# Kernel optimization log

Hardware: AMD Instinct MI355X
Metric: run time of the kernel (lower is better)

Reference implementation:

```python
import jax, jax.numpy as jnp
import numpy as np

N, H, HEADS, SLICES = 200000, 256, 8, 64
DH = H // HEADS  # 32


def setup_inputs() -> dict:
    key = jax.random.key(0)
    ks = jax.random.split(key, 13)
    r = lambda k, shape, scale: jax.random.normal(k, shape, dtype=jnp.float32) * scale
    return {
        "x": r(ks[0], (N, H), 1.0),
        "Wx": r(ks[1], (H, H), H ** -0.5),
        "bx": r(ks[2], (H,), 0.02),
        "Wfx": r(ks[3], (H, H), H ** -0.5),
        "bfx": r(ks[4], (H,), 0.02),
        "Wslice": r(ks[5], (SLICES, DH), DH ** -0.5),
        "bslice": r(ks[6], (SLICES,), 0.02),
        "Wq": r(ks[7], (DH, DH), DH ** -0.5),
        "Wk": r(ks[8], (DH, DH), DH ** -0.5),
        "Wv": r(ks[9], (DH, DH), DH ** -0.5),
        "Wout": r(ks[10], (H, H), H ** -0.5),
        "bout": r(ks[11], (H,), 0.02),
        "temperature": jnp.full((HEADS, 1, 1), 0.5, dtype=jnp.float32),
    }


def reference(x, Wx, bx, Wfx, bfx, Wslice, bslice, Wq, Wk, Wv, Wout, bout, temperature):
    n, hidden = x.shape
    heads, dh = HEADS, DH
    scale = dh ** -0.5

    def to_heads(y):  # (n, hidden) -> (heads, n, dh)
        return jnp.transpose(y.reshape(n, heads, dh), (1, 0, 2))

    fx_mid = to_heads(x @ Wfx.T + bfx)              # (h, n, d)
    x_mid = to_heads(x @ Wx.T + bx)                 # (h, n, d)

    temp = jnp.clip(temperature, 0.1, 5.0)          # (h, 1, 1)
    slice_logits = (jnp.einsum('hnd,gd->hng', x_mid, Wslice) + bslice) / temp
    slice_weights = jax.nn.softmax(slice_logits, axis=-1)   # (h, n, g)
    slice_norm = jnp.sum(slice_weights, axis=1)              # (h, g)

    slice_token = jnp.einsum('hnc,hng->hgc', fx_mid, slice_weights)
    slice_token = slice_token / (slice_norm[:, :, None] + 1e-05)  # (h, g, d)

    q = jnp.einsum('hgd,ed->hge', slice_token, Wq)
    k = jnp.einsum('hgd,ed->hge', slice_token, Wk)
    v = jnp.einsum('hgd,ed->hge', slice_token, Wv)

    dots = jnp.einsum('hgd,hkd->hgk', q, k) * scale
    attn = jax.nn.softmax(dots, axis=-1)
    out_slice = jnp.einsum('hgk,hkd->hgd', attn, v)          # (h, g, d)

    out_x = jnp.einsum('hgc,hng->hnc', out_slice, slice_weights)  # (h, n, d)
    out_x = jnp.transpose(out_x, (1, 0, 2)).reshape(n, hidden)
    return out_x @ Wout.T + bout
```

## Files before the change

kernel.cpp:

```cpp
#include <hip/hip_runtime.h>

typedef unsigned short u16;
typedef __attribute__((ext_vector_type(2))) unsigned int u32x2;
typedef __attribute__((ext_vector_type(4))) unsigned int u32x4;
typedef __attribute__((ext_vector_type(4))) float f32x4;
typedef __attribute__((ext_vector_type(8))) short bf16x8;

__device__ __forceinline__ float bf2f(u16 u) {
    union { unsigned int i; float f; } v; v.i = ((unsigned int)u) << 16; return v.f;
}
__device__ __forceinline__ u16 f2bf(float f) {
    union { float f; unsigned int i; } v; v.f = f;
    unsigned int x = v.i;
    return (u16)((x + 0x7fffu + ((x >> 16) & 1u)) >> 16);
}
__device__ __forceinline__ unsigned int pack2(float a, float b) {
    return (unsigned int)f2bf(a) | ((unsigned int)f2bf(b) << 16);
}
__device__ __forceinline__ void split2(float a, float b, unsigned int& h, unsigned int& l) {
    u16 ha = f2bf(a), hb = f2bf(b);
    u16 la = f2bf(a - bf2f(ha)), lb = f2bf(b - bf2f(hb));
    h = (unsigned int)ha | ((unsigned int)hb << 16);
    l = (unsigned int)la | ((unsigned int)lb << 16);
}
__device__ __forceinline__ void tsplit2(float a, float b,
                                        unsigned int& h, unsigned int& l) {
    unsigned int ua = __float_as_uint(a), ub = __float_as_uint(b);
    float fa = __uint_as_float(ua & 0xffff0000u);
    float fb = __uint_as_float(ub & 0xffff0000u);
    h = (ua >> 16) | (ub & 0xffff0000u);
    float la = a - fa, lb = b - fb;
    l = (__float_as_uint(la) >> 16) | (__float_as_uint(lb) & 0xffff0000u);
}

__device__ __forceinline__ f32x4 MFMA(bf16x8 a, bf16x8 b, f32x4 c) {
    return __builtin_amdgcn_mfma_f32_16x16x32_bf16(a, b, c, 0, 0, 0);
}

__global__ __launch_bounds__(256) void kprep(
    const float* __restrict__ Wx, const float* __restrict__ Wfx,
    const float* __restrict__ Wslice, const float* __restrict__ bslice,
    const float* __restrict__ temperature,
    u16* __restrict__ WxTb, u16* __restrict__ WfxTg,
    u16* __restrict__ WsP, float* __restrict__ bslv)
{
    const int gidx = blockIdx.x * 256 + threadIdx.x;
    if (gidx < 65536) {
        WxTb[gidx] = f2bf(Wx[gidx]);
    } else if (gidx < 131072) {
        const int i = gidx - 65536;
        WfxTg[i] = f2bf(Wfx[i]);
    } else if (gidx < 147456) {
        const int i = gidx - 131072;
        const int h = i >> 11;
        const int rem = i & 2047;
        const int gfc = rem >> 9;
        const int l = (rem >> 3) & 63;
        const int j = i & 7;
        const int g = gfc * 16 + (l & 15);
        const int d = ((j >> 2) << 4) + ((l >> 4) << 2) + (j & 3);
        float tc = fminf(fmaxf(temperature[h], 0.1f), 5.0f);
        WsP[i] = f2bf(Wslice[g * 32 + d] / tc);
    } else if (gidx < 147968) {
        const int i = gidx - 147456;
        const int h = i >> 6, g = i & 63;
        float tc = fminf(fmaxf(temperature[h], 0.1f), 5.0f);
        bslv[i] = bslice[g] / tc;
    }
}

#define LDS_XH 65536
#define LDS_XL 98304
#define LDS_IM 131072
__global__ __launch_bounds__(512, 2) void kAB(
    const float* __restrict__ x, const u16* __restrict__ WxTb,
    const u16* __restrict__ WfxTg, const u16* __restrict__ WsP,
    const float* __restrict__ bx, const float* __restrict__ bfx,
    const float* __restrict__ bslv,
    u16* __restrict__ swg, float* __restrict__ pst, float* __restrict__ pnorm)
{
    __shared__ char lds[147456];
    const int tid  = threadIdx.x;
    const int wv   = tid >> 6;
    const int lane = tid & 63;
    const int l15  = lane & 15;
    const int l4   = lane >> 4;
    const int hl   = wv >> 2;
    const int tq   = wv & 3;

    const int bid  = blockIdx.x;
    const int c    = bid >> 2;
    const int hp   = bid & 3;
    const int head = hp * 2 + hl;

    for (int u = tid; u < 4096; u += 512) {
        const int row = u >> 5, seg = u & 31;
        const u16* src;
        if (row < 64)
            src = WxTb + ((size_t)(hp * 2 + (row >> 5)) * 32 + (row & 31)) * 256 + seg * 8;
        else {
            const int rr = row - 64;
            src = WfxTg + ((size_t)(hp * 2 + (rr >> 5)) * 32 + (rr & 31)) * 256 + seg * 8;
        }
        *(u32x4*)(lds + ((row * 512 + seg * 16) ^ ((row & 7) << 4))) = *(const u32x4*)src;
    }

    bf16x8 wsp[4];
    #pragma unroll
    for (int g = 0; g < 4; ++g)
        wsp[g] = *(const bf16x8*)(WsP + (size_t)head * 2048 + g * 512 + lane * 8);
    float bsl[4], bfv[2], bxv[2][4];
    #pragma unroll
    for (int g = 0; g < 4; ++g) bsl[g] = bslv[head * 64 + g * 16 + l15];
    #pragma unroll
    for (int fc = 0; fc < 2; ++fc) bfv[fc] = bfx[head * 32 + fc * 16 + l15];
    #pragma unroll
    for (int fc = 0; fc < 2; ++fc)
        #pragma unroll
        for (int r = 0; r < 4; ++r)
            bxv[fc][r] = bx[head * 32 + fc * 16 + l4 * 4 + r];

    f32x4 stacc[2][4];
    #pragma unroll
    for (int i = 0; i < 2; ++i)
        #pragma unroll
        for (int j = 0; j < 4; ++j) stacc[i][j] = (f32x4){0.f, 0.f, 0.f, 0.f};
    float nacc[4] = {0.f, 0.f, 0.f, 0.f};

    const int cnt = 12 + (c < 53 ? 1 : 0);
    const long tb = (long)c * 12 + (c < 53 ? c : 53);

    const int row = tid >> 3, seg = tid & 7;
    const int xswz = (row & 7) << 4;

    f32x4 pf[8];
    #pragma unroll
    for (int i = 0; i < 8; ++i)
        pf[i] = *(const f32x4*)(x + (size_t)(tb * 64 + row) * 256 + i * 32 + seg * 4);

    const int xrow = tq * 16 + l15;
    const int xoff = xrow * 512;
    const int xkey = (xrow & 7) << 4;

    for (int t = 0; t < cnt; ++t) {
        const long tok0 = (tb + t) * 64;

        #pragma unroll
        for (int i = 0; i < 8; ++i) {
            unsigned int h0, l0, h1, l1;
            split2(pf[i][0], pf[i][1], h0, l0);
            split2(pf[i][2], pf[i][3], h1, l1);
            const int a = (row * 512 + i * 64 + seg * 8) ^ xswz;
            *(u32x2*)(lds + LDS_XH + a) = (u32x2){h0, h1};
            *(u32x2*)(lds + LDS_XL + a) = (u32x2){l0, l1};
        }
        __syncthreads();

        f32x4 acc1[2], accF[2];
        #pragma unroll
        for (int fc = 0; fc < 2; ++fc) {
            accF[fc] = (f32x4){bfv[fc], bfv[fc], bfv[fc], bfv[fc]};
            acc1[fc] = (f32x4){0.f, 0.f, 0.f, 0.f};
        }
        #pragma unroll
        for (int ks = 0; ks < 8; ++ks) {
            const int kb = ks * 64 + l4 * 16;
            bf16x8 ah = *(const bf16x8*)(lds + LDS_XH + ((xoff + kb) ^ xkey));
            bf16x8 al = *(const bf16x8*)(lds + LDS_XL + ((xoff + kb) ^ xkey));
            bf16x8 awx[2], awf[2];
            #pragma unroll
            for (int fc = 0; fc < 2; ++fc) {
                const int r1 = hl * 32 + fc * 16 + l15;
                awx[fc] = *(const bf16x8*)(lds + ((r1 * 512 + kb) ^ ((r1 & 7) << 4)));
                const int r2 = 64 + r1;
                awf[fc] = *(const bf16x8*)(lds + ((r2 * 512 + kb) ^ ((r2 & 7) << 4)));
            }
            #pragma unroll
            for (int fc = 0; fc < 2; ++fc) {
                accF[fc] = MFMA(ah, awf[fc], accF[fc]);
                acc1[fc] = MFMA(awx[fc], ah, acc1[fc]);
                acc1[fc] = MFMA(awx[fc], al, acc1[fc]);
            }
        }

        if (t + 1 < cnt) {
            #pragma unroll
            for (int i = 0; i < 8; ++i)
                pf[i] = *(const f32x4*)(x + (size_t)(tok0 + 64 + row) * 256 + i * 32 + seg * 4);
        }

        union { u32x4 u; bf16x8 b; } a2h, a2l;
        {
            unsigned int h0, l0, h1, l1, h2, l2, h3, l3;
            float m0 = acc1[0][0] + bxv[0][0];
            float m1 = acc1[0][1] + bxv[0][1];
            float m2 = acc1[0][2] + bxv[0][2];
            float m3 = acc1[0][3] + bxv[0][3];
            tsplit2(m0, m1, h0, l0);
            tsplit2(m2, m3, h1, l1);
            float n0 = acc1[1][0] + bxv[1][0];
            float n1 = acc1[1][1] + bxv[1][1];
            float n2 = acc1[1][2] + bxv[1][2];
            float n3 = acc1[1][3] + bxv[1][3];
            tsplit2(n0, n1, h2, l2);
            tsplit2(n2, n3, h3, l3);
            a2h.u = (u32x4){h0, h1, h2, h3};
            a2l.u = (u32x4){l0, l1, l2, l3};
        }
        f32x4 accL[4];
        #pragma unroll
        for (int g = 0; g < 4; ++g) {
            accL[g] = (f32x4){bsl[g], bsl[g], bsl[g], bsl[g]};
            accL[g] = MFMA(a2h.b, wsp[g], accL[g]);
            accL[g] = MFMA(a2l.b, wsp[g], accL[g]);
        }

        float mrow[4], srow4[4];
        #pragma unroll
        for (int r = 0; r < 4; ++r)
            mrow[r] = fmaxf(fmaxf(accL[0][r], accL[1][r]), fmaxf(accL[2][r], accL[3][r]));
        #pragma unroll
        for (int d = 1; d <= 8; d <<= 1)
            #pragma unroll
            for (int r = 0; r < 4; ++r)
                mrow[r] = fmaxf(mrow[r], __shfl_xor(mrow[r], d));
        #pragma unroll
        for (int r = 0; r < 4; ++r) {
            float e0 = __expf(accL[0][r] - mrow[r]);
            float e1 = __expf(accL[1][r] - mrow[r]);
            float e2 = __expf(accL[2][r] - mrow[r]);
            float e3 = __expf(accL[3][r] - mrow[r]);
            accL[0][r] = e0; accL[1][r] = e1; accL[2][r] = e2; accL[3][r] = e3;
            srow4[r] = e0 + e1 + e2 + e3;
        }
        #pragma unroll
        for (int d = 1; d <= 8; d <<= 1)
            #pragma unroll
            for (int r = 0; r < 4; ++r)
                srow4[r] += __shfl_xor(srow4[r], d);
        #pragma unroll
        for (int r = 0; r < 4; ++r) {
            const float inv = 1.0f / srow4[r];
            float e0 = accL[0][r] * inv, e1 = accL[1][r] * inv;
            float e2 = accL[2][r] * inv, e3 = accL[3][r] * inv;
            accL[0][r] = e0; accL[1][r] = e1; accL[2][r] = e2; accL[3][r] = e3;
            nacc[0] += e0; nacc[1] += e1; nacc[2] += e2; nacc[3] += e3;
        }

        unsigned int pL[4][2];
        #pragma unroll
        for (int fc = 0; fc < 4; ++fc) {
            u16 w0 = f2bf(accL[fc][0]), w1 = f2bf(accL[fc][1]);
            u16 w2 = f2bf(accL[fc][2]), w3 = f2bf(accL[fc][3]);
            pL[fc][0] = (unsigned int)w0 | ((unsigned int)w1 << 16);
            pL[fc][1] = (unsigned int)w2 | ((unsigned int)w3 << 16);
            const int col2 = (hl * 64 + fc * 16 + l15) * 2;
            #pragma unroll
            for (int r = 0; r < 4; ++r) {
                const int tok = tq * 16 + l4 * 4 + r;
                const int key = ((tok >> 2) & 3) << 5;
                const u16 val = (r == 0) ? w0 : (r == 1) ? w1 : (r == 2) ? w2 : w3;
                *(u16*)(lds + LDS_IM + ((tok * 256 + col2) ^ key)) = val;
            }
        }

        unsigned int pF[2][2];
        #pragma unroll
        for (int fc = 0; fc < 2; ++fc) {
            pF[fc][0] = pack2(accF[fc][0], accF[fc][1]);
            pF[fc][1] = pack2(accF[fc][2], accF[fc][3]);
        }
        #pragma unroll
        for (int mt2 = 0; mt2 < 2; ++mt2) {
            union { u32x4 u; bf16x8 b; } a;
            a.u = (u32x4){pF[mt2][0], pF[mt2][1], 0u, 0u};
            #pragma unroll
            for (int nt = 0; nt < 4; ++nt) {
                union { u32x4 u; bf16x8 b; } bb;
                bb.u = (u32x4){pL[nt][0], pL[nt][1], 0u, 0u};
                stacc[mt2][nt] = MFMA(a.b, bb.b, stacc[mt2][nt]);
            }
        }

        __syncthreads();

        #pragma unroll
        for (int q = 0; q < 2; ++q) {
            const int slot = q * 512 + tid;
            const int tok = slot >> 4, sg = slot & 15;
            const int key = ((tok >> 2) & 3) << 5;
            u32x4 v = *(const u32x4*)(lds + LDS_IM + ((tok * 256 + sg * 16) ^ key));
            __builtin_nontemporal_store(v,
                (u32x4*)(swg + (size_t)(tok0 + tok) * 512 + hp * 128 + sg * 8));
        }
    }

    __syncthreads();
    float* sst = (float*)lds;
    float* nst = (float*)(lds + LDS_IM);
    #pragma unroll
    for (int mt2 = 0; mt2 < 2; ++mt2)
        #pragma unroll
        for (int nt = 0; nt < 4; ++nt)
            #pragma unroll
            for (int r = 0; r < 4; ++r)
                sst[wv * 2048 + (mt2 * 16 + l4 * 4 + r) * 64 + nt * 16 + l15] = stacc[mt2][nt][r];
    #pragma unroll
    for (int fc = 0; fc < 4; ++fc) {
        float v = nacc[fc];
        v += __shfl_xor(v, 16); v += __shfl_xor(v, 32);
        if (l4 == 0) nst[wv * 64 + fc * 16 + l15] = v;
    }
    __syncthreads();
    for (int i = tid; i < 4096; i += 512) {
        const int hl2 = i >> 11, e = i & 2047;
        float s = sst[(hl2 * 4 + 0) * 2048 + e] + sst[(hl2 * 4 + 1) * 2048 + e]
                + sst[(hl2 * 4 + 2) * 2048 + e] + sst[(hl2 * 4 + 3) * 2048 + e];
        __builtin_nontemporal_store(s,
            pst + ((size_t)(hp * 2 + hl2) * 256 + c) * 2048 + e);
    }
    if (tid < 128) {
        const int hl2 = tid >> 6, g = tid & 63;
        float s = nst[(hl2 * 4 + 0) * 64 + g] + nst[(hl2 * 4 + 1) * 64 + g]
                + nst[(hl2 * 4 + 2) * 64 + g] + nst[(hl2 * 4 + 3) * 64 + g];
        pnorm[((size_t)(hp * 2 + hl2) * 256 + c) * 64 + g] = s;
    }
}

__global__ __launch_bounds__(256) void kC1(
    const float* __restrict__ pst, const float* __restrict__ pnorm,
    float* __restrict__ stn, float* __restrict__ norm)
{
    __shared__ float red[256];
    const int tid  = threadIdx.x;
    const int half = tid >> 7;
    const int li   = tid & 127;
    if (blockIdx.x < 128) {
        const int o  = blockIdx.x * 128 + li;
        const int h  = o >> 11, oo = o & 2047;
        float s = 0.f;
        for (int b = half * 128; b < half * 128 + 128; ++b)
            s += __builtin_nontemporal_load(pst + ((size_t)h * 256 + b) * 2048 + oo);
        red[tid] = s;
        __syncthreads();
        if (!half) stn[o] = red[li] + red[li + 128];
    } else {
        const int o = (blockIdx.x - 128) * 128 + li;
        const int h = o >> 6, g = o & 63;
        float s = 0.f;
        for (int b = half * 128; b < half * 128 + 128; ++b)
            s += pnorm[((size_t)h * 256 + b) * 64 + g];
        red[tid] = s;
        __syncthreads();
        if (!half) norm[o] = red[li] + red[li + 128];
    }
}

__global__ __launch_bounds__(64) void kattn(
    const float* __restrict__ stn, const float* __restrict__ norm,
    const float* __restrict__ Wq, const float* __restrict__ Wk,
    const float* __restrict__ Wv, float* __restrict__ os)
{
    __shared__ float kl[2048], vl[2048];
    const int h = blockIdx.x, g = threadIdx.x;
    const float ng = norm[h * 64 + g] + 1e-5f;
    float s[32];
    #pragma unroll
    for (int d = 0; d < 32; ++d) s[d] = stn[h * 2048 + d * 64 + g] / ng;
    float q[32];
    #pragma unroll
    for (int e = 0; e < 32; ++e) {
        float aq = 0.f, ak = 0.f, av = 0.f;
        #pragma unroll
        for (int d = 0; d < 32; ++d) {
            aq += s[d] * Wq[e * 32 + d];
            ak += s[d] * Wk[e * 32 + d];
            av += s[d] * Wv[e * 32 + d];
        }
        q[e] = aq; kl[g * 32 + e] = ak; vl[g * 32 + e] = av;
    }
    __syncthreads();
    float p[64];
    float mx = -1e30f;
    const float scale = 0.17677669529663689f;
    #pragma unroll
    for (int kk = 0; kk < 64; ++kk) {
        float a = 0.f;
        #pragma unroll
        for (int e = 0; e < 32; ++e) a += q[e] * kl[kk * 32 + e];
        a *= scale; p[kk] = a; mx = fmaxf(mx, a);
    }
    float sum = 0.f;
    #pragma unroll
    for (int kk = 0; kk < 64; ++kk) { p[kk] = __expf(p[kk] - mx); sum += p[kk]; }
    const float inv = 1.0f / sum;
    #pragma unroll
    for (int d = 0; d < 32; ++d) {
        float a = 0.f;
        #pragma unroll
        for (int kk = 0; kk < 64; ++kk) a += p[kk] * inv * vl[kk * 32 + d];
        os[h * 2048 + g * 32 + d] = a;
    }
}

__global__ __launch_bounds__(64) void kD2(
    const float* __restrict__ os, const float* __restrict__ Wout,
    u16* __restrict__ Wc2T)
{
    const int co = blockIdx.x;
    for (int rep = 0; rep < 8; ++rep) {
        const int hg = rep * 64 + threadIdx.x;
        const int h = hg >> 6, g = hg & 63;
        float s = 0.f;
        #pragma unroll
        for (int d = 0; d < 32; ++d)
            s += os[h * 2048 + g * 32 + d] * Wout[co * 256 + h * 32 + d];
        Wc2T[co * 512 + hg] = f2bf(s);
    }
}

__global__ __launch_bounds__(512, 2) void kE(
    const u16* __restrict__ swg, const u16* __restrict__ Wc2T,
    const float* __restrict__ bout, float* __restrict__ y)
{
    __shared__ char lds[65536];
    const int tid  = threadIdx.x;
    const int w    = tid >> 6;
    const int lane = tid & 63;
    const int l15  = lane & 15;
    const int l4   = lane >> 4;
    const int aswz = (l15 & 7) << 4;

    const int bid = blockIdx.x;
    const int cnt = 12 + (bid < 106 ? 1 : 0);
    const long tb = (long)bid * 12 + (bid < 106 ? bid : 106);

    bf16x8 Breg[16][2];
    #pragma unroll
    for (int ks = 0; ks < 16; ++ks)
        #pragma unroll
        for (int fc = 0; fc < 2; ++fc)
            Breg[ks][fc] = *(const bf16x8*)(Wc2T +
                (size_t)(w * 32 + fc * 16 + l15) * 512 + ks * 32 + l4 * 8);

    const float b0 = bout[w * 32 + l15], b1 = bout[w * 32 + 16 + l15];

    u32x4 pf[4];
    #pragma unroll
    for (int k = 0; k < 4; ++k) {
        const int slot = tid + k * 512;
        const int srow = slot >> 6, ss = slot & 63;
        pf[k] = __builtin_nontemporal_load(
            (const u32x4*)(swg + (size_t)(tb * 32 + srow) * 512 + ss * 8));
    }

    for (int t = 0; t < cnt; ++t) {
        const long tok0 = (tb + t) * 32;

        #pragma unroll
        for (int k = 0; k < 4; ++k) {
            const int slot = tid + k * 512;
            const int srow = slot >> 6, ss = slot & 63;
            *(u32x4*)(lds + ((srow * 1024 + ss * 16) ^ ((srow & 7) << 4))) = pf[k];
        }
        __syncthreads();

        if (t + 1 < cnt) {
            #pragma unroll
            for (int k = 0; k < 4; ++k) {
                const int slot = tid + k * 512;
                const int srow = slot >> 6, ss = slot & 63;
                pf[k] = __builtin_nontemporal_load(
                    (const u32x4*)(swg + (size_t)(tok0 + 32 + srow) * 512 + ss * 8));
            }
        }

        f32x4 acc[2][2];
        #pragma unroll
        for (int mt = 0; mt < 2; ++mt) {
            acc[mt][0] = (f32x4){b0, b0, b0, b0};
            acc[mt][1] = (f32x4){b1, b1, b1, b1};
        }

        #pragma unroll
        for (int ks = 0; ks < 16; ++ks) {
            bf16x8 a[2];
            #pragma unroll
            for (int mt = 0; mt < 2; ++mt)
                a[mt] = *(const bf16x8*)(lds + (mt * 16 + l15) * 1024 + ((ks * 64 + l4 * 16) ^ aswz));
            #pragma unroll
            for (int mt = 0; mt < 2; ++mt) {
                acc[mt][0] = MFMA(a[mt], Breg[ks][0], acc[mt][0]);
                acc[mt][1] = MFMA(a[mt], Breg[ks][1], acc[mt][1]);
            }
        }

        #pragma unroll
        for (int mt = 0; mt < 2; ++mt)
            #pragma unroll
            for (int fc = 0; fc < 2; ++fc)
                #pragma unroll
                for (int r = 0; r < 4; ++r) {
                    const int tok = mt * 16 + l4 * 4 + r;
                    const int col = w * 32 + fc * 16 + l15;
                    *(float*)(lds + 32768 + ((tok * 1024 + col * 4) ^ ((tok & 7) << 4))) =
                        acc[mt][fc][r];
                }
        __syncthreads();

        #pragma unroll
        for (int k = 0; k < 4; ++k) {
            const int slot = tid + k * 512;
            const int yrow = slot >> 6, ys = slot & 63;
            u32x4 v = *(const u32x4*)(lds + 32768 + ((yrow * 1024 + ys * 16) ^ ((yrow & 7) << 4)));
            __builtin_nontemporal_store(v,
                (u32x4*)(y + (size_t)(tok0 + yrow) * 256 + ys * 4));
        }
    }
}

extern "C" void kernel_launch(void* const* d_in, const int* in_sizes, int n_in,
                              void* d_out, int out_size, void* d_ws, size_t ws_size,
                              hipStream_t stream) {
    const float* x       = (const float*)d_in[0];
    const float* Wx      = (const float*)d_in[1];
    const float* bx      = (const float*)d_in[2];
    const float* Wfx     = (const float*)d_in[3];
    const float* bfx     = (const float*)d_in[4];
    const float* Wslice  = (const float*)d_in[5];
    const float* bslice  = (const float*)d_in[6];
    const float* Wq      = (const float*)d_in[7];
    const float* Wk      = (const float*)d_in[8];
    const float* Wv      = (const float*)d_in[9];
    const float* Wout    = (const float*)d_in[10];
    const float* bout    = (const float*)d_in[11];
    const float* temp    = (const float*)d_in[12];

    char* wsb = (char*)d_ws;
    u16*   sw    = (u16*)(wsb);
    float* pst   = (float*)(wsb + 204800000);
    float* pnorm = (float*)(wsb + 238354432);
    u16*   WxTb  = (u16*)(wsb + 239403008);
    u16*   WfxTg = (u16*)(wsb + 239534080);
    u16*   WsP   = (u16*)(wsb + 239665152);
    float* bslv  = (float*)(wsb + 239697920);
    u16*   Wc2T  = (u16*)(wsb + 239798272);
    float* os    = (float*)(wsb + 240060416);
    float* stn   = (float*)(wsb + 240125952);
    float* norm  = (float*)(wsb + 240191488);
    float* y     = (float*)d_out;

    kprep<<<578, 256, 0, stream>>>(Wx, Wfx, Wslice, bslice, temp, WxTb, WfxTg, WsP, bslv);
    kAB<<<1024, 512, 0, stream>>>(x, WxTb, WfxTg, WsP, bx, bfx, bslv, sw, pst, pnorm);
    kC1<<<132, 256, 0, stream>>>(pst, pnorm, stn, norm);
    kattn<<<8, 64, 0, stream>>>(stn, norm, Wq, Wk, Wv, os);
    kD2<<<256, 64, 0, stream>>>(os, Wout, Wc2T);
    kE<<<512, 512, 0, stream>>>(sw, Wc2T, bout, y);
}
```

Measured before the change: 539.0 us.

## Load kE A-operand directly from global and double-buffer the output staging LDS

```diff
diff --git a/kernel.cpp b/kernel.cpp
--- a/kernel.cpp
+++ b/kernel.cpp
@@ -429,7 +429,6 @@
     const int lane = tid & 63;
     const int l15  = lane & 15;
     const int l4   = lane >> 4;
-    const int aswz = (l15 & 7) << 4;
 
     const int bid = blockIdx.x;
     const int cnt = 12 + (bid < 106 ? 1 : 0);
@@ -445,54 +444,25 @@
 
     const float b0 = bout[w * 32 + l15], b1 = bout[w * 32 + 16 + l15];
 
-    u32x4 pf[4];
-    #pragma unroll
-    for (int k = 0; k < 4; ++k) {
-        const int slot = tid + k * 512;
-        const int srow = slot >> 6, ss = slot & 63;
-        pf[k] = __builtin_nontemporal_load(
-            (const u32x4*)(swg + (size_t)(tb * 32 + srow) * 512 + ss * 8));
-    }
-
     for (int t = 0; t < cnt; ++t) {
         const long tok0 = (tb + t) * 32;
-
-        #pragma unroll
-        for (int k = 0; k < 4; ++k) {
-            const int slot = tid + k * 512;
-            const int srow = slot >> 6, ss = slot & 63;
-            *(u32x4*)(lds + ((srow * 1024 + ss * 16) ^ ((srow & 7) << 4))) = pf[k];
-        }
-        __syncthreads();
-
-        if (t + 1 < cnt) {
-            #pragma unroll
-            for (int k = 0; k < 4; ++k) {
-                const int slot = tid + k * 512;
-                const int srow = slot >> 6, ss = slot & 63;
-                pf[k] = __builtin_nontemporal_load(
-                    (const u32x4*)(swg + (size_t)(tok0 + 32 + srow) * 512 + ss * 8));
-            }
-        }
+        char* img = lds + ((t & 1) << 15);
 
         f32x4 acc[2][2];
-        #pragma unroll
-        for (int mt = 0; mt < 2; ++mt) {
-            acc[mt][0] = (f32x4){b0, b0, b0, b0};
-            acc[mt][1] = (f32x4){b1, b1, b1, b1};
-        }
-
+        acc[0][0] = (f32x4){b0, b0, b0, b0};
+        acc[0][1] = (f32x4){b1, b1, b1, b1};
+        acc[1][0] = (f32x4){b0, b0, b0, b0};
+        acc[1][1] = (f32x4){b1, b1, b1, b1};
+
+        const u16* Ap = swg + ((size_t)tok0 + l15) * 512 + l4 * 8;
         #pragma unroll
         for (int ks = 0; ks < 16; ++ks) {
-            bf16x8 a[2];
-            #pragma unroll
-            for (int mt = 0; mt < 2; ++mt)
-                a[mt] = *(const bf16x8*)(lds + (mt * 16 + l15) * 1024 + ((ks * 64 + l4 * 16) ^ aswz));
-            #pragma unroll
-            for (int mt = 0; mt < 2; ++mt) {
-                acc[mt][0] = MFMA(a[mt], Breg[ks][0], acc[mt][0]);
-                acc[mt][1] = MFMA(a[mt], Breg[ks][1], acc[mt][1]);
-            }
+            bf16x8 a0 = *(const bf16x8*)(Ap + ks * 32);
+            bf16x8 a1 = *(const bf16x8*)(Ap + (size_t)16 * 512 + ks * 32);
+            acc[0][0] = MFMA(a0, Breg[ks][0], acc[0][0]);
+            acc[0][1] = MFMA(a0, Breg[ks][1], acc[0][1]);
+            acc[1][0] = MFMA(a1, Breg[ks][0], acc[1][0]);
+            acc[1][1] = MFMA(a1, Breg[ks][1], acc[1][1]);
         }
 
         #pragma unroll
@@ -503,7 +473,7 @@
                 for (int r = 0; r < 4; ++r) {
                     const int tok = mt * 16 + l4 * 4 + r;
                     const int col = w * 32 + fc * 16 + l15;
-                    *(float*)(lds + 32768 + ((tok * 1024 + col * 4) ^ ((tok & 7) << 4))) =
+                    *(float*)(img + ((tok * 1024 + col * 4) ^ ((tok & 7) << 4))) =
                         acc[mt][fc][r];
                 }
         __syncthreads();
@@ -512,7 +482,7 @@
         for (int k = 0; k < 4; ++k) {
             const int slot = tid + k * 512;
             const int yrow = slot >> 6, ys = slot & 63;
-            u32x4 v = *(const u32x4*)(lds + 32768 + ((yrow * 1024 + ys * 16) ^ ((yrow & 7) << 4)));
+            u32x4 v = *(const u32x4*)(img + ((yrow * 1024 + ys * 16) ^ ((yrow & 7) << 4)));
             __builtin_nontemporal_store(v,
                 (u32x4*)(y + (size_t)(tok0 + yrow) * 256 + ys * 4));
         }
```

Measured after the change: 714.1 us. +32.5%, slower.
